# Kernel tuning notes

Measured on AMD Instinct MI355X. Metric: run time of the kernel, lower is better.

## Reference

```python
import jax, jax.numpy as jnp
import numpy as np
import math

B, S, D, H = 8, 2048, 1024, 16
DH = D // H  # attention head size = 64

def setup_inputs() -> dict:
    key = jax.random.key(0)
    ks = jax.random.split(key, 10)
    s = 1.0 / math.sqrt(D)
    return {
        "hidden_states": jax.random.normal(ks[0], (B, S, D), dtype=jnp.float32),
        "attention_mask": jnp.zeros((B, 1, S), dtype=jnp.float32),
        "Wq": jax.random.normal(ks[1], (D, D), dtype=jnp.float32) * s,
        "bq": jnp.zeros((D,), dtype=jnp.float32),
        "Wqa": jax.random.normal(ks[2], (D, H), dtype=jnp.float32) * s,
        "bqa": jnp.zeros((H,), dtype=jnp.float32),
        "Wk": jax.random.normal(ks[3], (D, D), dtype=jnp.float32) * s,
        "bk": jnp.zeros((D,), dtype=jnp.float32),
        "Wt": jax.random.normal(ks[4], (D, D), dtype=jnp.float32) * s,
        "bt": jnp.zeros((D,), dtype=jnp.float32),
    }

def reference(hidden_states, attention_mask, Wq, bq, Wqa, bqa, Wk, bk, Wt, bt):
    scale = 1.0 / math.sqrt(DH)
    q = hidden_states @ Wq + bq                      # [B,S,D] mixed_query_layer
    k = hidden_states @ Wk + bk                      # [B,S,D] mixed_key_layer
    # query attention logits -> [B,H,S]
    q_score = jnp.swapaxes(q @ Wqa + bqa, 1, 2) * scale + attention_mask
    q_weight = jax.nn.softmax(q_score, axis=-1)      # [B,H,S]
    ql = jnp.swapaxes(q.reshape(B, S, H, DH), 1, 2)  # [B,H,S,DH]
    kl = jnp.swapaxes(k.reshape(B, S, H, DH), 1, 2)  # [B,H,S,DH]
    pooled_q = jnp.einsum('bhs,bhsd->bhd', q_weight, ql)          # [B,H,DH]
    qk_score = jnp.einsum('bhsd,bhd->bhs', kl, pooled_q) * scale + attention_mask
    qk_weight = jax.nn.softmax(qk_score, axis=-1)                 # [B,H,S]
    pooled_k = jnp.einsum('bhs,bhsd->bhd', qk_weight, kl)         # [B,H,DH]
    weighted = pooled_k[:, :, None, :] * ql                       # [B,H,S,DH]
    weighted = jnp.swapaxes(weighted, 1, 2).reshape(B, S, D)      # [B,S,D]
    out = weighted @ Wt + bt + q                                  # transform + residual to query
    return out
```

## Files before the change

kernel.cpp:

```cpp
#include <hip/hip_runtime.h>
#include <hip/hip_bf16.h>
#include <math.h>

#define BB 8
#define SS 2048
#define DD 1024
#define HH 16
#define DHH 64
#define NROWS (BB*SS)
#define QSLICE ((size_t)BB * HH * SS)

typedef unsigned short u16;
typedef __attribute__((ext_vector_type(8))) __bf16 bf16x8;
typedef __attribute__((ext_vector_type(4))) float f32x4;

__device__ __forceinline__ u16 f2bf(float f) {
    union { float f; unsigned u; } v; v.f = f;
    unsigned r = v.u + 0x7fffu + ((v.u >> 16) & 1u);
    return (u16)(r >> 16);
}
__device__ __forceinline__ float bf2f(u16 b) {
    union { unsigned u; float f; } v; v.u = ((unsigned)b) << 16;
    return v.f;
}

__device__ __forceinline__ void load_lds16(const void* g, void* l) {
    __builtin_amdgcn_global_load_lds(
        (const __attribute__((address_space(1))) unsigned int*)g,
        (__attribute__((address_space(3))) unsigned int*)l,
        16, 0, 0);
}

#define BAR() do { asm volatile("" ::: "memory"); \
                   __builtin_amdgcn_s_barrier();  \
                   asm volatile("" ::: "memory"); } while (0)

__global__ __launch_bounds__(256)
void prep_kernel(const float* __restrict__ hs, u16* __restrict__ hs_bf,
                 const float* __restrict__ Wq, u16* __restrict__ WqT,
                 const float* __restrict__ Wk, u16* __restrict__ WkT,
                 const float* __restrict__ Wt, u16* __restrict__ WtT,
                 const float* __restrict__ Wqa, u16* __restrict__ WqaT) {
    __shared__ float tile[32][33];
    const int bid = blockIdx.x;
    const int t = threadIdx.x;
    if (bid < 16384) {
        int i = bid * 256 + t;
        float4 v = ((const float4*)hs)[i];
        ushort4 o;
        o.x = f2bf(v.x); o.y = f2bf(v.y); o.z = f2bf(v.z); o.w = f2bf(v.w);
        ((ushort4*)hs_bf)[i] = o;
        return;
    }
    if (bid < 19456) {
        int rel = bid - 16384;
        const float* W; u16* WT;
        if (rel < 1024)      { W = Wq; WT = WqT; }
        else if (rel < 2048) { W = Wk; WT = WkT; rel -= 1024; }
        else                 { W = Wt; WT = WtT; rel -= 2048; }
        int m0 = (rel & 31) * 32, k0 = (rel >> 5) * 32;
        int tx = t & 31, ty = t >> 5;
        #pragma unroll
        for (int i = 0; i < 4; i++) {
            int kk = ty + i * 8;
            tile[kk][tx] = W[(k0 + kk) * DD + m0 + tx];
        }
        __syncthreads();
        #pragma unroll
        for (int i = 0; i < 4; i++) {
            int mm = ty + i * 8;
            WT[(m0 + mm) * DD + k0 + tx] = f2bf(tile[tx][mm]);
        }
        return;
    }
    {
        int i = (bid - 19456) * 256 + t;
        int h = i >> 10, k = i & 1023;
        WqaT[i] = f2bf(Wqa[k * HH + h]);
    }
}

template<int MODE>
__global__ __launch_bounds__(512, 2)
void gemm256_kernel(const u16* __restrict__ A, const u16* __restrict__ BT,
                    const float* __restrict__ b0, const float* __restrict__ b1,
                    const u16* __restrict__ res, float* __restrict__ Cf,
                    u16* __restrict__ C0, u16* __restrict__ C1,
                    const u16* __restrict__ WqaT, float* __restrict__ qraw) {
    __shared__ u16 smem[69632];
    const int by = blockIdx.y;
    const int row0 = blockIdx.x * 256;
    const int bcol0 = by * 256;
    const int colg0 = (MODE == 1) ? (bcol0 & 1023) : bcol0;
    const float* bias = (MODE == 1 && by >= 4) ? b1 : b0;
    u16* Cb = (MODE == 1 && by >= 4) ? C1 : C0;
    const u16* BTb = (MODE == 2) ? BT + ((size_t)(row0 >> 11) << 20) : BT;

    const int t = threadIdx.x;
    const int w = t >> 6, lane = t & 63;
    const int wm = w >> 2, wn = w & 3;
    const int m16 = lane & 15, quad = lane >> 4;

    f32x4 acc[8][4];
    #pragma unroll
    for (int i = 0; i < 8; i++)
        #pragma unroll
        for (int j = 0; j < 4; j++)
            acc[i][j] = (f32x4){0.f, 0.f, 0.f, 0.f};

    const int srow = t >> 3;
    const int scol = ((t & 7) ^ (srow & 7)) * 8;
    const u16* Ag = A + (size_t)(row0 + srow) * DD + scol;
    const u16* Bg = BTb + (size_t)(bcol0 + srow) * DD + scol;

    auto STAGE_H = [&](int ktile, int mat, int half) {
        if (ktile >= 16) return;
        const int buf = ktile & 1;
        const int k0 = ktile * 64;
        const u16* g = mat ? Bg : Ag;
        u16* s = smem + mat * 32768 + buf * 16384;
        #pragma unroll
        for (int j = 0; j < 2; ++j)
            load_lds16(g + k0 + (size_t)(half * 128 + j * 64) * DD,
                       s + half * 8192 + j * 4096 + t * 8);
    };

    STAGE_H(0, 0, 0); STAGE_H(0, 0, 1); STAGE_H(0, 1, 0); STAGE_H(0, 1, 1);
    STAGE_H(1, 0, 0);
    asm volatile("s_waitcnt vmcnt(2)" ::: "memory");
    BAR();

    for (int kt = 0; kt < 16; ++kt) {
        const int cur = kt & 1;
        const u16* sAc = smem + cur * 16384;
        const u16* sBc = smem + 32768 + cur * 16384;
        bf16x8 af[4][2], bfr[4][2];

        #pragma unroll
        for (int mi = 0; mi < 4; ++mi)
            #pragma unroll
            for (int ks = 0; ks < 2; ++ks)
                af[mi][ks] = *(const bf16x8*)&sAc[(wm * 128 + mi * 16 + m16) * 64 +
                                                 (((ks * 4 + quad) ^ (m16 & 7)) * 8)];
        #pragma unroll
        for (int ni = 0; ni < 2; ++ni)
            #pragma unroll
            for (int ks = 0; ks < 2; ++ks)
                bfr[ni][ks] = *(const bf16x8*)&sBc[(wn * 64 + ni * 16 + m16) * 64 +
                                                   (((ks * 4 + quad) ^ (m16 & 7)) * 8)];
        STAGE_H(kt + 1, 0, 1);
        BAR();
        __builtin_amdgcn_s_setprio(1);
        #pragma unroll
        for (int mi = 0; mi < 4; ++mi)
            #pragma unroll
            for (int ni = 0; ni < 2; ++ni)
                #pragma unroll
                for (int ks = 0; ks < 2; ++ks)
                    acc[mi][ni] = __builtin_amdgcn_mfma_f32_16x16x32_bf16(
                        bfr[ni][ks], af[mi][ks], acc[mi][ni], 0, 0, 0);
        __builtin_amdgcn_s_setprio(0);
        BAR();

        #pragma unroll
        for (int ni = 2; ni < 4; ++ni)
            #pragma unroll
            for (int ks = 0; ks < 2; ++ks)
                bfr[ni][ks] = *(const bf16x8*)&sBc[(wn * 64 + ni * 16 + m16) * 64 +
                                                   (((ks * 4 + quad) ^ (m16 & 7)) * 8)];
        STAGE_H(kt + 1, 1, 0);
        BAR();
        __builtin_amdgcn_s_setprio(1);
        #pragma unroll
        for (int mi = 0; mi < 4; ++mi)
            #pragma unroll
            for (int ni = 2; ni < 4; ++ni)
                #pragma unroll
                for (int ks = 0; ks < 2; ++ks)
                    acc[mi][ni] = __builtin_amdgcn_mfma_f32_16x16x32_bf16(
                        bfr[ni][ks], af[mi][ks], acc[mi][ni], 0, 0, 0);
        __builtin_amdgcn_s_setprio(0);
        BAR();

        #pragma unroll
        for (int mi = 0; mi < 4; ++mi)
            #pragma unroll
            for (int ks = 0; ks < 2; ++ks)
                af[mi][ks] = *(const bf16x8*)&sAc[(wm * 128 + (4 + mi) * 16 + m16) * 64 +
                                                 (((ks * 4 + quad) ^ (m16 & 7)) * 8)];
        STAGE_H(kt + 1, 1, 1);
        BAR();
        __builtin_amdgcn_s_setprio(1);
        #pragma unroll
        for (int mi = 0; mi < 4; ++mi)
            #pragma unroll
            for (int ni = 0; ni < 2; ++ni)
                #pragma unroll
                for (int ks = 0; ks < 2; ++ks)
                    acc[4 + mi][ni] = __builtin_amdgcn_mfma_f32_16x16x32_bf16(
                        bfr[ni][ks], af[mi][ks], acc[4 + mi][ni], 0, 0, 0);
        __builtin_amdgcn_s_setprio(0);
        BAR();

        STAGE_H(kt + 2, 0, 0);
        BAR();
        __builtin_amdgcn_s_setprio(1);
        #pragma unroll
        for (int mi = 0; mi < 4; ++mi)
            #pragma unroll
            for (int ni = 2; ni < 4; ++ni)
                #pragma unroll
                for (int ks = 0; ks < 2; ++ks)
                    acc[4 + mi][ni] = __builtin_amdgcn_mfma_f32_16x16x32_bf16(
                        bfr[ni][ks], af[mi][ks], acc[4 + mi][ni], 0, 0, 0);
        __builtin_amdgcn_s_setprio(0);
        if (kt < 14) asm volatile("s_waitcnt vmcnt(2)" ::: "memory");
        else         asm volatile("s_waitcnt vmcnt(0)" ::: "memory");
        BAR();
    }

    u16* sC = smem;
    #pragma unroll
    for (int mi = 0; mi < 8; ++mi) {
        const int lrow = wm * 128 + mi * 16 + m16;
        #pragma unroll
        for (int ni = 0; ni < 4; ++ni) {
            const int lcol = wn * 64 + ni * 16 + quad * 4;
            const float4 bv = *(const float4*)&bias[colg0 + lcol];
            if (MODE == 1) {
                ushort4 o;
                o.x = f2bf(acc[mi][ni][0] + bv.x);
                o.y = f2bf(acc[mi][ni][1] + bv.y);
                o.z = f2bf(acc[mi][ni][2] + bv.z);
                o.w = f2bf(acc[mi][ni][3] + bv.w);
                *(ushort4*)&sC[(size_t)lrow * 272 + lcol] = o;
            } else {
                const size_t idx = (size_t)(row0 + lrow) * DD + colg0 + lcol;
                const ushort4 rv = *(const ushort4*)&res[idx];
                float4 o;
                o.x = acc[mi][ni][0] + bv.x + bf2f(rv.x);
                o.y = acc[mi][ni][1] + bv.y + bf2f(rv.y);
                o.z = acc[mi][ni][2] + bv.z + bf2f(rv.z);
                o.w = acc[mi][ni][3] + bv.w + bf2f(rv.w);
                *(float4*)&Cf[idx] = o;
            }
        }
    }
    if (MODE == 1) {
        __syncthreads();
        #pragma unroll
        for (int it = 0; it < 16; ++it) {
            const int r = it * 16 + (t >> 5);
            const int c = t & 31;
            uint4 v = *(const uint4*)&sC[(size_t)r * 272 + c * 8];
            *(uint4*)&Cb[(size_t)(row0 + r) * DD + colg0 + c * 8] = v;
        }
        if (by < 4) {
            const int bIdx = row0 >> 11;
            bf16x8 wq[8];
            const u16* bp = WqaT + (size_t)m16 * DD + by * 256 + quad * 8;
            #pragma unroll
            for (int kk = 0; kk < 8; ++kk) wq[kk] = *(const bf16x8*)(bp + kk * 32);
            #pragma unroll
            for (int rt = 0; rt < 2; ++rt) {
                const int sr = (w * 2 + rt) * 16;
                f32x4 qa = (f32x4){0.f, 0.f, 0.f, 0.f};
                #pragma unroll
                for (int kk = 0; kk < 8; ++kk) {
                    bf16x8 a = *(const bf16x8*)&sC[(size_t)(sr + m16) * 272 + quad * 8 + kk * 32];
                    qa = __builtin_amdgcn_mfma_f32_16x16x32_bf16(a, wq[kk], qa, 0, 0, 0);
                }
                #pragma unroll
                for (int r = 0; r < 4; ++r) {
                    int s = (row0 & 2047) + sr + quad * 4 + r;
                    qraw[((size_t)(by * BB + bIdx) * HH + m16) * SS + s] = qa[r];
                }
            }
        }
    }
}

__global__ __launch_bounds__(512)
void attnmid_kernel(const float* __restrict__ qraw, const float* __restrict__ bqa,
                    const float* __restrict__ mask, const u16* __restrict__ qbf,
                    const u16* __restrict__ kbf, float* __restrict__ pk) {
    const int bh = blockIdx.x;
    const int b = bh >> 4, h = bh & 15;
    const int t = threadIdx.x;
    const int wid = t >> 6, lane = t & 63;
    __shared__ float sw[SS];
    __shared__ float red[8];
    __shared__ float prr[8][64];
    __shared__ float pql[64];

    {
        const float* qr = qraw + ((size_t)bh << 11);
        float v[4]; float m = -1e30f;
        #pragma unroll
        for (int i = 0; i < 4; i++) {
            int off = t + i * 512;
            float x = qr[off] + qr[off + QSLICE] + qr[off + 2 * QSLICE] + qr[off + 3 * QSLICE];
            x = (x + bqa[h]) * 0.125f + mask[b * SS + off];
            v[i] = x; m = fmaxf(m, x);
        }
        #pragma unroll
        for (int o = 32; o; o >>= 1) m = fmaxf(m, __shfl_xor(m, o));
        if (lane == 0) red[wid] = m;
        __syncthreads();
        m = red[0];
        #pragma unroll
        for (int i = 1; i < 8; i++) m = fmaxf(m, red[i]);
        float sum = 0.f;
        #pragma unroll
        for (int i = 0; i < 4; i++) { v[i] = __expf(v[i] - m); sum += v[i]; }
        #pragma unroll
        for (int o = 32; o; o >>= 1) sum += __shfl_xor(sum, o);
        __syncthreads();
        if (lane == 0) red[wid] = sum;
        __syncthreads();
        float tot = 0.f;
        #pragma unroll
        for (int i = 0; i < 8; i++) tot += red[i];
        float inv = 1.0f / tot;
        #pragma unroll
        for (int i = 0; i < 4; i++) sw[t + i * 512] = v[i] * inv;
        __syncthreads();
    }

    {
        const int d0 = (lane & 31) * 2;
        const int srel = lane >> 5;
        const u16* base = qbf + (((size_t)b * SS) << 10) + h * 64 + d0;
        float a0 = 0.f, a1 = 0.f;
        #pragma unroll 8
        for (int it = 0; it < 128; ++it) {
            int s = wid * 256 + it * 2 + srel;
            unsigned kw = *(const unsigned*)(base + ((size_t)s << 10));
            float wf = sw[s];
            union { unsigned u; float f; } lo, hi;
            lo.u = kw << 16; hi.u = kw & 0xffff0000u;
            a0 += wf * lo.f; a1 += wf * hi.f;
        }
        a0 += __shfl_xor(a0, 32); a1 += __shfl_xor(a1, 32);
        if (lane < 32) { prr[wid][d0] = a0; prr[wid][d0 + 1] = a1; }
        __syncthreads();
        if (t < 64) {
            float s2 = 0.f;
            #pragma unroll
            for (int w2 = 0; w2 < 8; w2++) s2 += prr[w2][t];
            pql[t] = s2;
        }
        __syncthreads();
    }

    {
        float v[4]; float m = -1e30f;
        #pragma unroll
        for (int i = 0; i < 4; i++) {
            int s = t + i * 512;
            const uint4* kp = (const uint4*)(kbf + (((size_t)(b * SS + s)) << 10) + h * 64);
            float acc = 0.f;
            #pragma unroll
            for (int j = 0; j < 8; j++) {
                uint4 kv = kp[j];
                unsigned ww[4] = {kv.x, kv.y, kv.z, kv.w};
                #pragma unroll
                for (int q2 = 0; q2 < 4; q2++) {
                    union { unsigned u; float f; } lo, hi;
                    lo.u = ww[q2] << 16; hi.u = ww[q2] & 0xffff0000u;
                    acc += lo.f * pql[j * 8 + q2 * 2] + hi.f * pql[j * 8 + q2 * 2 + 1];
                }
            }
            float x = acc * 0.125f + mask[b * SS + s];
            v[i] = x; m = fmaxf(m, x);
        }
        #pragma unroll
        for (int o = 32; o; o >>= 1) m = fmaxf(m, __shfl_xor(m, o));
        __syncthreads();
        if (lane == 0) red[wid] = m;
        __syncthreads();
        m = red[0];
        #pragma unroll
        for (int i = 1; i < 8; i++) m = fmaxf(m, red[i]);
        float sum = 0.f;
        #pragma unroll
        for (int i = 0; i < 4; i++) { v[i] = __expf(v[i] - m); sum += v[i]; }
        #pragma unroll
        for (int o = 32; o; o >>= 1) sum += __shfl_xor(sum, o);
        __syncthreads();
        if (lane == 0) red[wid] = sum;
        __syncthreads();
        float tot = 0.f;
        #pragma unroll
        for (int i = 0; i < 8; i++) tot += red[i];
        float inv = 1.0f / tot;
        #pragma unroll
        for (int i = 0; i < 4; i++) sw[t + i * 512] = v[i] * inv;
        __syncthreads();
    }

    {
        const int d0 = (lane & 31) * 2;
        const int srel = lane >> 5;
        const u16* base = kbf + (((size_t)b * SS) << 10) + h * 64 + d0;
        float a0 = 0.f, a1 = 0.f;
        #pragma unroll 8
        for (int it = 0; it < 128; ++it) {
            int s = wid * 256 + it * 2 + srel;
            unsigned kw = *(const unsigned*)(base + ((size_t)s << 10));
            float wf = sw[s];
            union { unsigned u; float f; } lo, hi;
            lo.u = kw << 16; hi.u = kw & 0xffff0000u;
            a0 += wf * lo.f; a1 += wf * hi.f;
        }
        a0 += __shfl_xor(a0, 32); a1 += __shfl_xor(a1, 32);
        if (lane < 32) { prr[wid][d0] = a0; prr[wid][d0 + 1] = a1; }
        __syncthreads();
        if (t < 64) {
            float s2 = 0.f;
            #pragma unroll
            for (int w2 = 0; w2 < 8; w2++) s2 += prr[w2][t];
            pk[b * DD + h * 64 + t] = s2;
        }
    }
}

__global__ __launch_bounds__(256)
void wtscale_kernel(const u16* __restrict__ WtT, const float* __restrict__ pk,
                    u16* __restrict__ WtT8) {
    size_t i = (size_t)blockIdx.x * 256 + threadIdx.x;
    int b = (int)(i >> 17);
    size_t off = (i & 131071) << 3;
    int d = (int)(off & 1023);
    const float4 p0 = *(const float4*)&pk[b * 1024 + d];
    const float4 p1 = *(const float4*)&pk[b * 1024 + d + 4];
    ushort4 a0 = ((const ushort4*)(WtT + off))[0];
    ushort4 a1 = ((const ushort4*)(WtT + off))[1];
    ushort4 o0, o1;
    o0.x = f2bf(bf2f(a0.x) * p0.x); o0.y = f2bf(bf2f(a0.y) * p0.y);
    o0.z = f2bf(bf2f(a0.z) * p0.z); o0.w = f2bf(bf2f(a0.w) * p0.w);
    o1.x = f2bf(bf2f(a1.x) * p1.x); o1.y = f2bf(bf2f(a1.y) * p1.y);
    o1.z = f2bf(bf2f(a1.z) * p1.z); o1.w = f2bf(bf2f(a1.w) * p1.w);
    u16* dst = WtT8 + ((size_t)b << 20) + off;
    ((ushort4*)dst)[0] = o0;
    ((ushort4*)dst)[1] = o1;
}

extern "C" void kernel_launch(void* const* d_in, const int* in_sizes, int n_in,
                              void* d_out, int out_size, void* d_ws, size_t ws_size,
                              hipStream_t stream) {
    const float* hs   = (const float*)d_in[0];
    const float* mask = (const float*)d_in[1];
    const float* Wq   = (const float*)d_in[2];
    const float* bq   = (const float*)d_in[3];
    const float* Wqa  = (const float*)d_in[4];
    const float* bqa  = (const float*)d_in[5];
    const float* Wk   = (const float*)d_in[6];
    const float* bk   = (const float*)d_in[7];
    const float* Wt   = (const float*)d_in[8];
    const float* bt   = (const float*)d_in[9];
    float* out = (float*)d_out;

    char* ws = (char*)d_ws;
    u16*   hs_bf = (u16*)ws;   ws += (size_t)NROWS * DD * 2;
    u16*   WqT   = (u16*)ws;   ws += (size_t)DD * DD * 2;
    u16*   WkT   = (u16*)ws;   ws += (size_t)DD * DD * 2;
    u16*   WtT   = (u16*)ws;   ws += (size_t)DD * DD * 2;
    u16*   WqaT  = (u16*)ws;   ws += (size_t)HH * DD * 2;
    u16*   q_bf  = (u16*)ws;   ws += (size_t)NROWS * DD * 2;
    u16*   k_bf  = (u16*)ws;   ws += (size_t)NROWS * DD * 2;
    float* qraw  = (float*)ws; ws += QSLICE * 4 * 4;
    float* pk    = (float*)ws; ws += (size_t)BB * HH * 64 * 4;
    u16*   WtT8  = hs_bf;

    prep_kernel<<<19520, 256, 0, stream>>>(hs, hs_bf, Wq, WqT, Wk, WkT, Wt, WtT,
                                           Wqa, WqaT);

    gemm256_kernel<1><<<dim3(NROWS / 256, 8), 512, 0, stream>>>(
        hs_bf, WqT, bq, bk, nullptr, nullptr, q_bf, k_bf, WqaT, qraw);

    attnmid_kernel<<<BB * HH, 512, 0, stream>>>(qraw, bqa, mask, q_bf, k_bf, pk);

    wtscale_kernel<<<4096, 256, 0, stream>>>(WtT, pk, WtT8);

    gemm256_kernel<2><<<dim3(NROWS / 256, 4), 512, 0, stream>>>(
        q_bf, WtT8, bt, nullptr, q_bf, out, nullptr, nullptr, nullptr, nullptr);
}
```

Measured before the change: 285.1 us.

## Restructure attention-pooling kernel with 1024 threads and 16-byte coalesced loads

The mid attention kernel now runs 1024 threads per block. Each group of 8 lanes reads a full 128-byte head row with uint4 loads, where it previously used 4-byte loads, and the per-row dot products are reduced with shuffles. The QK score pass switches from one thread per row reading 128 bytes serially to 8 lanes cooperating per row, which improves coalescing and memory-level parallelism in this kernel, which has only 128 blocks. It adds more shuffle reductions and an extra sync, and it uses the larger block size to expose more parallelism on a grid that is too small to fill the device.

```diff
diff --git a/kernel.cpp b/kernel.cpp
--- a/kernel.cpp
+++ b/kernel.cpp
@@ -280,7 +280,7 @@
     }
 }
 
-__global__ __launch_bounds__(512)
+__global__ __launch_bounds__(1024)
 void attnmid_kernel(const float* __restrict__ qraw, const float* __restrict__ bqa,
                     const float* __restrict__ mask, const u16* __restrict__ qbf,
                     const u16* __restrict__ kbf, float* __restrict__ pk) {
@@ -288,138 +288,159 @@
     const int b = bh >> 4, h = bh & 15;
     const int t = threadIdx.x;
     const int wid = t >> 6, lane = t & 63;
+    const int sub = lane & 7;
+    const int srw = lane >> 3;
+
     __shared__ float sw[SS];
-    __shared__ float red[8];
-    __shared__ float prr[8][64];
+    __shared__ float redM[16], redS[16];
+    __shared__ float prr[16][64];
     __shared__ float pql[64];
 
     {
         const float* qr = qraw + ((size_t)bh << 11);
-        float v[4]; float m = -1e30f;
-        #pragma unroll
-        for (int i = 0; i < 4; i++) {
-            int off = t + i * 512;
-            float x = qr[off] + qr[off + QSLICE] + qr[off + 2 * QSLICE] + qr[off + 3 * QSLICE];
-            x = (x + bqa[h]) * 0.125f + mask[b * SS + off];
-            v[i] = x; m = fmaxf(m, x);
-        }
+        const float bq_ = bqa[h];
+        float x0 = qr[t] + qr[t + QSLICE] + qr[t + 2 * QSLICE] + qr[t + 3 * QSLICE];
+        float x1 = qr[t + 1024] + qr[t + 1024 + QSLICE] + qr[t + 1024 + 2 * QSLICE]
+                 + qr[t + 1024 + 3 * QSLICE];
+        x0 = (x0 + bq_) * 0.125f + mask[b * SS + t];
+        x1 = (x1 + bq_) * 0.125f + mask[b * SS + t + 1024];
+        float m = fmaxf(x0, x1);
         #pragma unroll
         for (int o = 32; o; o >>= 1) m = fmaxf(m, __shfl_xor(m, o));
-        if (lane == 0) red[wid] = m;
-        __syncthreads();
-        m = red[0];
-        #pragma unroll
-        for (int i = 1; i < 8; i++) m = fmaxf(m, red[i]);
-        float sum = 0.f;
-        #pragma unroll
-        for (int i = 0; i < 4; i++) { v[i] = __expf(v[i] - m); sum += v[i]; }
+        if (lane == 0) redM[wid] = m;
+        __syncthreads();
+        m = redM[0];
+        #pragma unroll
+        for (int i = 1; i < 16; i++) m = fmaxf(m, redM[i]);
+        float e0 = __expf(x0 - m), e1 = __expf(x1 - m);
+        float sum = e0 + e1;
         #pragma unroll
         for (int o = 32; o; o >>= 1) sum += __shfl_xor(sum, o);
-        __syncthreads();
-        if (lane == 0) red[wid] = sum;
+        if (lane == 0) redS[wid] = sum;
         __syncthreads();
         float tot = 0.f;
         #pragma unroll
-        for (int i = 0; i < 8; i++) tot += red[i];
+        for (int i = 0; i < 16; i++) tot += redS[i];
         float inv = 1.0f / tot;
-        #pragma unroll
-        for (int i = 0; i < 4; i++) sw[t + i * 512] = v[i] * inv;
+        sw[t] = e0 * inv;
+        sw[t + 1024] = e1 * inv;
         __syncthreads();
     }
 
     {
-        const int d0 = (lane & 31) * 2;
-        const int srel = lane >> 5;
-        const u16* base = qbf + (((size_t)b * SS) << 10) + h * 64 + d0;
-        float a0 = 0.f, a1 = 0.f;
-        #pragma unroll 8
-        for (int it = 0; it < 128; ++it) {
-            int s = wid * 256 + it * 2 + srel;
-            unsigned kw = *(const unsigned*)(base + ((size_t)s << 10));
+        const u16* qb = qbf + (((size_t)b * SS) << 10) + h * 64 + sub * 8;
+        float a[8];
+        #pragma unroll
+        for (int j = 0; j < 8; j++) a[j] = 0.f;
+        #pragma unroll
+        for (int it = 0; it < 16; ++it) {
+            int s = it * 128 + wid * 8 + srw;
+            uint4 kv = *(const uint4*)(qb + ((size_t)s << 10));
             float wf = sw[s];
-            union { unsigned u; float f; } lo, hi;
-            lo.u = kw << 16; hi.u = kw & 0xffff0000u;
-            a0 += wf * lo.f; a1 += wf * hi.f;
-        }
-        a0 += __shfl_xor(a0, 32); a1 += __shfl_xor(a1, 32);
-        if (lane < 32) { prr[wid][d0] = a0; prr[wid][d0 + 1] = a1; }
+            unsigned ww[4] = {kv.x, kv.y, kv.z, kv.w};
+            #pragma unroll
+            for (int j = 0; j < 4; j++) {
+                union { unsigned u; float f; } lo, hi;
+                lo.u = ww[j] << 16; hi.u = ww[j] & 0xffff0000u;
+                a[2 * j]     += wf * lo.f;
+                a[2 * j + 1] += wf * hi.f;
+            }
+        }
+        #pragma unroll
+        for (int o = 8; o <= 32; o <<= 1)
+            #pragma unroll
+            for (int j = 0; j < 8; j++) a[j] += __shfl_xor(a[j], o);
+        if (srw == 0)
+            #pragma unroll
+            for (int j = 0; j < 8; j++) prr[wid][sub * 8 + j] = a[j];
         __syncthreads();
         if (t < 64) {
             float s2 = 0.f;
             #pragma unroll
-            for (int w2 = 0; w2 < 8; w2++) s2 += prr[w2][t];
+            for (int w2 = 0; w2 < 16; w2++) s2 += prr[w2][t];
             pql[t] = s2;
         }
         __syncthreads();
     }
 
     {
-        float v[4]; float m = -1e30f;
-        #pragma unroll
-        for (int i = 0; i < 4; i++) {
-            int s = t + i * 512;
-            const uint4* kp = (const uint4*)(kbf + (((size_t)(b * SS + s)) << 10) + h * 64);
-            float acc = 0.f;
-            #pragma unroll
-            for (int j = 0; j < 8; j++) {
-                uint4 kv = kp[j];
-                unsigned ww[4] = {kv.x, kv.y, kv.z, kv.w};
-                #pragma unroll
-                for (int q2 = 0; q2 < 4; q2++) {
-                    union { unsigned u; float f; } lo, hi;
-                    lo.u = ww[q2] << 16; hi.u = ww[q2] & 0xffff0000u;
-                    acc += lo.f * pql[j * 8 + q2 * 2] + hi.f * pql[j * 8 + q2 * 2 + 1];
-                }
+        const u16* kb = kbf + (((size_t)b * SS) << 10) + h * 64 + sub * 8;
+        float pqr[8];
+        #pragma unroll
+        for (int j = 0; j < 8; j++) pqr[j] = pql[sub * 8 + j];
+        #pragma unroll
+        for (int it = 0; it < 16; ++it) {
+            int s = it * 128 + wid * 8 + srw;
+            uint4 kv = *(const uint4*)(kb + ((size_t)s << 10));
+            unsigned ww[4] = {kv.x, kv.y, kv.z, kv.w};
+            float d = 0.f;
+            #pragma unroll
+            for (int j = 0; j < 4; j++) {
+                union { unsigned u; float f; } lo, hi;
+                lo.u = ww[j] << 16; hi.u = ww[j] & 0xffff0000u;
+                d += lo.f * pqr[2 * j] + hi.f * pqr[2 * j + 1];
             }
-            float x = acc * 0.125f + mask[b * SS + s];
-            v[i] = x; m = fmaxf(m, x);
-        }
+            d += __shfl_xor(d, 1);
+            d += __shfl_xor(d, 2);
+            d += __shfl_xor(d, 4);
+            if (sub == 0) sw[s] = d * 0.125f + mask[b * SS + s];
+        }
+        __syncthreads();
+        float x0 = sw[t], x1 = sw[t + 1024];
+        float m = fmaxf(x0, x1);
         #pragma unroll
         for (int o = 32; o; o >>= 1) m = fmaxf(m, __shfl_xor(m, o));
-        __syncthreads();
-        if (lane == 0) red[wid] = m;
-        __syncthreads();
-        m = red[0];
-        #pragma unroll
-        for (int i = 1; i < 8; i++) m = fmaxf(m, red[i]);
-        float sum = 0.f;
-        #pragma unroll
-        for (int i = 0; i < 4; i++) { v[i] = __expf(v[i] - m); sum += v[i]; }
+        if (lane == 0) redM[wid] = m;
+        __syncthreads();
+        m = redM[0];
+        #pragma unroll
+        for (int i = 1; i < 16; i++) m = fmaxf(m, redM[i]);
+        float e0 = __expf(x0 - m), e1 = __expf(x1 - m);
+        float sum = e0 + e1;
         #pragma unroll
         for (int o = 32; o; o >>= 1) sum += __shfl_xor(sum, o);
-        __syncthreads();
-        if (lane == 0) red[wid] = sum;
+        if (lane == 0) redS[wid] = sum;
         __syncthreads();
         float tot = 0.f;
         #pragma unroll
-        for (int i = 0; i < 8; i++) tot += red[i];
+        for (int i = 0; i < 16; i++) tot += redS[i];
         float inv = 1.0f / tot;
-        #pragma unroll
-        for (int i = 0; i < 4; i++) sw[t + i * 512] = v[i] * inv;
+        sw[t] = e0 * inv;
+        sw[t + 1024] = e1 * inv;
         __syncthreads();
     }
 
     {
-        const int d0 = (lane & 31) * 2;
-        const int srel = lane >> 5;
-        const u16* base = kbf + (((size_t)b * SS) << 10) + h * 64 + d0;
-        float a0 = 0.f, a1 = 0.f;
-        #pragma unroll 8
-        for (int it = 0; it < 128; ++it) {
-            int s = wid * 256 + it * 2 + srel;
-            unsigned kw = *(const unsigned*)(base + ((size_t)s << 10));
+        const u16* kb = kbf + (((size_t)b * SS) << 10) + h * 64 + sub * 8;
+        float a[8];
+        #pragma unroll
+        for (int j = 0; j < 8; j++) a[j] = 0.f;
+        #pragma unroll
+        for (int it = 0; it < 16; ++it) {
+            int s = it * 128 + wid * 8 + srw;
+            uint4 kv = *(const uint4*)(kb + ((size_t)s << 10));
             float wf = sw[s];
-            union { unsigned u; float f; } lo, hi;
-            lo.u = kw << 16; hi.u = kw & 0xffff0000u;
-            a0 += wf * lo.f; a1 += wf * hi.f;
-        }
-        a0 += __shfl_xor(a0, 32); a1 += __shfl_xor(a1, 32);
-        if (lane < 32) { prr[wid][d0] = a0; prr[wid][d0 + 1] = a1; }
+            unsigned ww[4] = {kv.x, kv.y, kv.z, kv.w};
+            #pragma unroll
+            for (int j = 0; j < 4; j++) {
+                union { unsigned u; float f; } lo, hi;
+                lo.u = ww[j] << 16; hi.u = ww[j] & 0xffff0000u;
+                a[2 * j]     += wf * lo.f;
+                a[2 * j + 1] += wf * hi.f;
+            }
+        }
+        #pragma unroll
+        for (int o = 8; o <= 32; o <<= 1)
+            #pragma unroll
+            for (int j = 0; j < 8; j++) a[j] += __shfl_xor(a[j], o);
+        if (srw == 0)
+            #pragma unroll
+            for (int j = 0; j < 8; j++) prr[wid][sub * 8 + j] = a[j];
         __syncthreads();
         if (t < 64) {
             float s2 = 0.f;
             #pragma unroll
-            for (int w2 = 0; w2 < 8; w2++) s2 += prr[w2][t];
+            for (int w2 = 0; w2 < 16; w2++) s2 += prr[w2][t];
             pk[b * DD + h * 64 + t] = s2;
         }
     }
@@ -479,7 +500,7 @@
     gemm256_kernel<1><<<dim3(NROWS / 256, 8), 512, 0, stream>>>(
         hs_bf, WqT, bq, bk, nullptr, nullptr, q_bf, k_bf, WqaT, qraw);
 
-    attnmid_kernel<<<BB * HH, 512, 0, stream>>>(qraw, bqa, mask, q_bf, k_bf, pk);
+    attnmid_kernel<<<BB * HH, 1024, 0, stream>>>(qraw, bqa, mask, q_bf, k_bf, pk);
 
     wtscale_kernel<<<4096, 256, 0, stream>>>(WtT, pk, WtT8);
 
```

Measured after the change: 275.2 us. 1.04x faster.
